# Kernel tuning notes

Measured on AMD Instinct MI355X. Metric: run time of the kernel, lower is better.

## Reference

```python
import jax, jax.numpy as jnp
import numpy as np

NUM_EMBEDDINGS = 8192
EMBEDDING_DIM = 256
COMMITMENT_COST = 0.25


def setup_inputs() -> dict:
    key = jax.random.key(0)
    k1, k2 = jax.random.split(key)
    z_e = jax.random.normal(k1, (16, 2048, EMBEDDING_DIM), dtype=jnp.float32)
    # nn.Embedding init: uniform(-1/K, 1/K)
    codebook = jax.random.uniform(
        k2, (NUM_EMBEDDINGS, EMBEDDING_DIM), dtype=jnp.float32,
        minval=-1.0 / NUM_EMBEDDINGS, maxval=1.0 / NUM_EMBEDDINGS)
    return {"z_e": z_e, "codebook": codebook}


def _nearest_indices(z_flat, codebook):
    # squared euclidean distances; argmin is identical to argmin of cdist
    # z_flat: [T, D], codebook: [K, D] -> dist2: [T, K]
    x2 = jnp.sum(z_flat * z_flat, axis=-1, keepdims=True)          # [T, 1]
    w2 = jnp.sum(codebook * codebook, axis=-1)                      # [K]
    xw = jnp.einsum('td,kd->tk', z_flat, codebook)                  # [T, K]
    dist2 = x2 - 2.0 * xw + w2
    return jnp.argmin(dist2, axis=1)                                # [T]


def reference(z_e, codebook):
    original_shape = z_e.shape
    z_e_flat = z_e.reshape(-1, EMBEDDING_DIM)
    indices = _nearest_indices(z_e_flat, codebook)
    z_q = codebook[indices].reshape(original_shape)
    # straight-through estimator
    z_q_ste = z_e + jax.lax.stop_gradient(z_q - z_e)
    commitment_loss = jnp.mean((z_e - jax.lax.stop_gradient(z_q_ste)) ** 2)
    codebook_loss = jnp.mean((z_q_ste - jax.lax.stop_gradient(z_e)) ** 2)
    loss = codebook_loss + COMMITMENT_COST * commitment_loss
    # codebook usage: fraction of unique indices (jit-friendly via scatter)
    used = jnp.zeros((NUM_EMBEDDINGS,), dtype=jnp.float32).at[indices].set(1.0)
    usage = jnp.sum(used) / NUM_EMBEDDINGS
    return (z_q_ste, loss, usage)
```

## Files before the change

### kernel.cpp

```cpp
#include <hip/hip_runtime.h>
#include <float.h>

#define T_TOTAL 32768
#define KC      8192
#define DIM     256

#define LOSS_IDX  ((size_t)T_TOTAL * DIM)
#define USAGE_IDX (LOSS_IDX + 1)

typedef short s16x8 __attribute__((ext_vector_type(8)));
typedef float f32x4 __attribute__((ext_vector_type(4)));

#define WS_W2    0
#define WS_FLAGS 32768
#define WS_CBF   65536

__device__ __forceinline__ unsigned short f2bf(float f) {
    unsigned int u = __float_as_uint(f);
    u += 0x7FFFu + ((u >> 16) & 1u);
    return (unsigned short)(u >> 16);
}

__global__ __launch_bounds__(256) void vq_prep(const float* __restrict__ cb,
                                               unsigned short* __restrict__ cbb,
                                               float* __restrict__ w2,
                                               int* __restrict__ flags,
                                               float* __restrict__ out) {
    const int blk = blockIdx.x, tid = threadIdx.x;
    size_t i = (size_t)blk * 2048 + (size_t)tid * 8;
    float4 a = *(const float4*)(cb + i);
    float4 b = *(const float4*)(cb + i + 4);
    uint4 o;
    o.x = (unsigned)f2bf(a.x) | ((unsigned)f2bf(a.y) << 16);
    o.y = (unsigned)f2bf(a.z) | ((unsigned)f2bf(a.w) << 16);
    o.z = (unsigned)f2bf(b.x) | ((unsigned)f2bf(b.y) << 16);
    o.w = (unsigned)f2bf(b.z) | ((unsigned)f2bf(b.w) << 16);
    *(uint4*)(cbb + i) = o;
    float s = a.x * a.x + a.y * a.y + a.z * a.z + a.w * a.w
            + b.x * b.x + b.y * b.y + b.z * b.z + b.w * b.w;
    #pragma unroll
    for (int m = 1; m <= 16; m <<= 1) s += __shfl_xor(s, m);
    if ((tid & 31) == 0) w2[blk * 8 + (tid >> 5)] = s;
    if (blk < 32) flags[blk * 256 + tid] = 0;
    if (blk == 0 && tid == 0) { out[LOSS_IDX] = 0.0f; out[USAGE_IDX] = 0.0f; }
}

__global__ __launch_bounds__(512, 2) void vq_main(const unsigned short* __restrict__ cbb,
                                                  const float* __restrict__ w2g,
                                                  const float* __restrict__ z_e,
                                                  const float* __restrict__ cb,
                                                  float* __restrict__ out,
                                                  int* __restrict__ flags) {
    __shared__ unsigned short ca[8][4][2048];
    __shared__ unsigned long long smin[128];
    __shared__ float wls[8];

    const int tid  = threadIdx.x;
    const int lane = tid & 63;
    const int w    = tid >> 6;
    const int wr   = w >> 2;
    const int wc   = w & 3;
    const int quad = lane >> 4;
    const int l15  = lane & 15;
    const int t0   = blockIdx.x * 128;

    if (tid < 128) smin[tid] = ~0ULL;
    __syncthreads();

    const int srow = lane >> 3;
    const int ssl  = lane & 7;
    const unsigned short* pstage = cbb + (wc * 32 + srow) * DIM + (ssl ^ srow) * 8;

    #define STAGE(PC, KW, BP)                                                           \
        {                                                                               \
            _Pragma("unroll")                                                           \
            for (int q = 0; q < 4; ++q) {                                               \
                __builtin_amdgcn_global_load_lds(                                       \
                    (const __attribute__((address_space(1))) void*)((PC) + (KW) * 64 + q * 2048), \
                    (__attribute__((address_space(3))) void*)(&ca[w][BP][q * 512]),     \
                    16, 0, 0);                                                          \
            }                                                                           \
        }

    const unsigned short* fragp[4];
    #pragma unroll
    for (int kk = 0; kk < 2; ++kk)
        #pragma unroll
        for (int j = 0; j < 2; ++j) {
            int row = j * 16 + l15;
            int sl = (kk * 4 + quad) ^ (l15 & 7);
            fragp[kk * 2 + j] = &ca[w][0][row * 64 + sl * 8];
        }

    #define READFRAGS(FB, BP)                                                           \
        {                                                                               \
            _Pragma("unroll")                                                           \
            for (int f = 0; f < 4; ++f)                                                 \
                (FB)[f] = *(const s16x8*)(fragp[f] + (BP) * 2048);                      \
        }

    STAGE(pstage, 0, 0); STAGE(pstage, 1, 1); STAGE(pstage, 2, 2); STAGE(pstage, 3, 3);
    s16x8 af[4][8];
    #pragma unroll
    for (int i = 0; i < 4; ++i) {
        #pragma unroll
        for (int ks = 0; ks < 8; ++ks) {
            const float* p = z_e + (size_t)(t0 + wr * 64 + i * 16 + l15) * DIM + ks * 32 + quad * 8;
            float4 a = *(const float4*)p;
            float4 b = *(const float4*)(p + 4);
            s16x8 v;
            v[0] = (short)f2bf(a.x); v[1] = (short)f2bf(a.y);
            v[2] = (short)f2bf(a.z); v[3] = (short)f2bf(a.w);
            v[4] = (short)f2bf(b.x); v[5] = (short)f2bf(b.y);
            v[6] = (short)f2bf(b.z); v[7] = (short)f2bf(b.w);
            af[i][ks] = v;
        }
    }

    float best[4][4];
    int   bidx[4][4];
    #pragma unroll
    for (int i = 0; i < 4; ++i)
        #pragma unroll
        for (int r = 0; r < 4; ++r) { best[i][r] = FLT_MAX; bidx[i][r] = 0x7FFFFFFF; }

    const float* pw2 = w2g + wc * 32 + l15;

    s16x8 regB[2][4];
    __builtin_amdgcn_s_waitcnt(0x0F7C);
    READFRAGS(regB[0], 0);

    for (int c = 0; c < 64; ++c) {
        f32x4 acc[4][2];
        #pragma unroll
        for (int i = 0; i < 4; ++i)
            #pragma unroll
            for (int j = 0; j < 2; ++j) acc[i][j] = (f32x4){0.f, 0.f, 0.f, 0.f};

        const unsigned short* pcn = pstage + ((size_t)((c + 1) & 63) << 15);

        #pragma unroll
        for (int kw = 0; kw < 4; ++kw) {
            __builtin_amdgcn_s_waitcnt(0xC07F);
            STAGE(pcn, kw, kw);
            __builtin_amdgcn_s_waitcnt(0x0F78);
            READFRAGS(regB[(kw + 1) & 1], (kw + 1) & 3);
            const s16x8* cur = regB[kw & 1];
            __builtin_amdgcn_s_setprio(1);
            #pragma unroll
            for (int kk = 0; kk < 2; ++kk)
                #pragma unroll
                for (int i = 0; i < 4; ++i)
                    #pragma unroll
                    for (int j = 0; j < 2; ++j)
                        acc[i][j] = __builtin_amdgcn_mfma_f32_16x16x32_bf16(af[i][kw * 2 + kk], cur[kk * 2 + j], acc[i][j], 0, 0, 0);
            __builtin_amdgcn_s_setprio(0);
        }

        #pragma unroll
        for (int j = 0; j < 2; ++j) {
            int col = c * 128 + wc * 32 + j * 16 + l15;
            float w2v = pw2[c * 128 + j * 16];
            #pragma unroll
            for (int i = 0; i < 4; ++i)
                #pragma unroll
                for (int r = 0; r < 4; ++r) {
                    float s = fmaf(-2.0f, acc[i][j][r], w2v);
                    if (s < best[i][r]) { best[i][r] = s; bidx[i][r] = col; }
                }
        }
    }

    #pragma unroll
    for (int i = 0; i < 4; ++i)
        #pragma unroll
        for (int r = 0; r < 4; ++r) {
            float b = best[i][r]; int ix = bidx[i][r];
            #pragma unroll
            for (int m = 1; m < 16; m <<= 1) {
                float ob = __shfl_xor(b, m);
                int   oi = __shfl_xor(ix, m);
                if (ob < b || (ob == b && oi < ix)) { b = ob; ix = oi; }
            }
            if (l15 == 0) {
                unsigned int fb = __float_as_uint(b);
                fb = (fb & 0x80000000u) ? ~fb : (fb | 0x80000000u);
                unsigned long long key = ((unsigned long long)fb << 32) | (unsigned int)ix;
                atomicMin(&smin[wr * 64 + i * 16 + quad * 4 + r], key);
            }
        }
    __syncthreads();

    float lsum = 0.0f;
    for (int t = w * 16; t < w * 16 + 16; ++t) {
        int tok = t0 + t;
        int k = (int)(unsigned int)(smin[t] & 0xFFFFFFFFull);
        if (lane == 0) flags[k] = 1;
        float4 cv = *(const float4*)(cb + (size_t)k * DIM + lane * 4);
        float4 zv = *(const float4*)(z_e + (size_t)tok * DIM + lane * 4);
        float dx = zv.x - cv.x, dy = zv.y - cv.y, dz = zv.z - cv.z, dw = zv.w - cv.w;
        lsum += dx * dx + dy * dy + dz * dz + dw * dw;
        *(float4*)(out + (size_t)tok * DIM + lane * 4) = cv;
    }
    #pragma unroll
    for (int m = 32; m >= 1; m >>= 1) lsum += __shfl_xor(lsum, m);
    if (lane == 0) wls[w] = lsum;
    __syncthreads();
    if (tid == 0) {
        float bsum = 0.0f;
        #pragma unroll
        for (int q = 0; q < 8; ++q) bsum += wls[q];
        atomicAdd(out + LOSS_IDX, bsum * (1.25f / (float)LOSS_IDX));
    }
}

__global__ __launch_bounds__(256) void vq_usage(const int* __restrict__ flags,
                                                float* __restrict__ out) {
    __shared__ int ws[4];
    int tid = threadIdx.x;
    int s = 0;
    for (int i = tid; i < KC; i += 256) s += flags[i];
    #pragma unroll
    for (int m = 32; m >= 1; m >>= 1) s += __shfl_xor(s, m);
    if ((tid & 63) == 0) ws[tid >> 6] = s;
    __syncthreads();
    if (tid == 0) out[USAGE_IDX] = (float)(ws[0] + ws[1] + ws[2] + ws[3]) / (float)KC;
}

extern "C" void kernel_launch(void* const* d_in, const int* in_sizes, int n_in,
                              void* d_out, int out_size, void* d_ws, size_t ws_size,
                              hipStream_t stream) {
    (void)in_sizes; (void)n_in; (void)out_size; (void)ws_size;
    const float* z_e = (const float*)d_in[0];
    const float* cb  = (const float*)d_in[1];
    float* out = (float*)d_out;

    char* ws = (char*)d_ws;
    float* w2    = (float*)(ws + WS_W2);
    int*   flags = (int*)(ws + WS_FLAGS);
    unsigned short* cbb = (unsigned short*)(ws + WS_CBF);

    vq_prep<<<KC / 8, 256, 0, stream>>>(cb, cbb, w2, flags, out);
    vq_main<<<T_TOTAL / 128, 512, 0, stream>>>(cbb, w2, z_e, cb, out, flags);
    vq_usage<<<1, 256, 0, stream>>>(flags, out);
}
```

Measured before the change: 243.1 us.

## Share codebook LDS tiles between wave pairs and cache w2 in shared memory

Waves with the same column group now load half of each codebook tile cooperatively into a shared LDS buffer, rather than every wave staging its own full copy. This halves global-to-LDS traffic and the LDS footprint. Block-wide barriers are added after every k-step so the shared buffers are not overwritten while still being read. The w2 norms for all codes are preloaded into LDS so per-chunk global loads disappear. The cost is a barrier per k-step, which can stall waves that would otherwise run independently.

```diff
diff --git a/kernel.cpp b/kernel.cpp
--- a/kernel.cpp
+++ b/kernel.cpp
@@ -51,7 +51,8 @@
                                                   const float* __restrict__ cb,
                                                   float* __restrict__ out,
                                                   int* __restrict__ flags) {
-    __shared__ unsigned short ca[8][4][2048];
+    __shared__ unsigned short ca[4][4][2048];
+    __shared__ float w2s[KC];
     __shared__ unsigned long long smin[128];
     __shared__ float wls[8];
 
@@ -65,21 +66,23 @@
     const int t0   = blockIdx.x * 128;
 
     if (tid < 128) smin[tid] = ~0ULL;
-    __syncthreads();
 
     const int srow = lane >> 3;
     const int ssl  = lane & 7;
-    const unsigned short* pstage = cbb + (wc * 32 + srow) * DIM + (ssl ^ srow) * 8;
+    const unsigned short* pstage =
+        cbb + (size_t)(wc * 32 + wr * 16 + srow) * DIM + (ssl ^ srow) * 8;
+    unsigned short* lb = &ca[wc][0][wr * 1024];
 
     #define STAGE(PC, KW, BP)                                                           \
         {                                                                               \
-            _Pragma("unroll")                                                           \
-            for (int q = 0; q < 4; ++q) {                                               \
-                __builtin_amdgcn_global_load_lds(                                       \
-                    (const __attribute__((address_space(1))) void*)((PC) + (KW) * 64 + q * 2048), \
-                    (__attribute__((address_space(3))) void*)(&ca[w][BP][q * 512]),     \
-                    16, 0, 0);                                                          \
-            }                                                                           \
+            __builtin_amdgcn_global_load_lds(                                           \
+                (const __attribute__((address_space(1))) void*)((PC) + (KW) * 64),      \
+                (__attribute__((address_space(3))) void*)(lb + (BP) * 2048),            \
+                16, 0, 0);                                                              \
+            __builtin_amdgcn_global_load_lds(                                           \
+                (const __attribute__((address_space(1))) void*)((PC) + (KW) * 64 + 2048), \
+                (__attribute__((address_space(3))) void*)(lb + (BP) * 2048 + 512),      \
+                16, 0, 0);                                                              \
         }
 
     const unsigned short* fragp[4];
@@ -89,7 +92,7 @@
         for (int j = 0; j < 2; ++j) {
             int row = j * 16 + l15;
             int sl = (kk * 4 + quad) ^ (l15 & 7);
-            fragp[kk * 2 + j] = &ca[w][0][row * 64 + sl * 8];
+            fragp[kk * 2 + j] = &ca[wc][0][row * 64 + sl * 8];
         }
 
     #define READFRAGS(FB, BP)                                                           \
@@ -100,6 +103,11 @@
         }
 
     STAGE(pstage, 0, 0); STAGE(pstage, 1, 1); STAGE(pstage, 2, 2); STAGE(pstage, 3, 3);
+    {
+        const float4* s = (const float4*)w2g + tid * 4;
+        float4* d = (float4*)w2s + tid * 4;
+        d[0] = s[0]; d[1] = s[1]; d[2] = s[2]; d[3] = s[3];
+    }
     s16x8 af[4][8];
     #pragma unroll
     for (int i = 0; i < 4; ++i) {
@@ -124,11 +132,14 @@
         #pragma unroll
         for (int r = 0; r < 4; ++r) { best[i][r] = FLT_MAX; bidx[i][r] = 0x7FFFFFFF; }
 
-    const float* pw2 = w2g + wc * 32 + l15;
+    const float* pw2s = &w2s[wc * 32 + l15];
 
     s16x8 regB[2][4];
-    __builtin_amdgcn_s_waitcnt(0x0F7C);
+    __builtin_amdgcn_s_waitcnt(0x0F70);
+    __syncthreads();
     READFRAGS(regB[0], 0);
+    __builtin_amdgcn_s_waitcnt(0xC07F);
+    __builtin_amdgcn_s_barrier();
 
     for (int c = 0; c < 64; ++c) {
         f32x4 acc[4][2];
@@ -141,9 +152,8 @@
 
         #pragma unroll
         for (int kw = 0; kw < 4; ++kw) {
-            __builtin_amdgcn_s_waitcnt(0xC07F);
             STAGE(pcn, kw, kw);
-            __builtin_amdgcn_s_waitcnt(0x0F78);
+            __builtin_amdgcn_s_waitcnt(0x0F74);
             READFRAGS(regB[(kw + 1) & 1], (kw + 1) & 3);
             const s16x8* cur = regB[kw & 1];
             __builtin_amdgcn_s_setprio(1);
@@ -155,12 +165,14 @@
                     for (int j = 0; j < 2; ++j)
                         acc[i][j] = __builtin_amdgcn_mfma_f32_16x16x32_bf16(af[i][kw * 2 + kk], cur[kk * 2 + j], acc[i][j], 0, 0, 0);
             __builtin_amdgcn_s_setprio(0);
+            __builtin_amdgcn_s_waitcnt(0xC07F);
+            __builtin_amdgcn_s_barrier();
         }
 
         #pragma unroll
         for (int j = 0; j < 2; ++j) {
             int col = c * 128 + wc * 32 + j * 16 + l15;
-            float w2v = pw2[c * 128 + j * 16];
+            float w2v = pw2s[c * 128 + j * 16];
             #pragma unroll
             for (int i = 0; i < 4; ++i)
                 #pragma unroll
```

New measurement: 253.5 us. 1.04x slower.

## Share staged codebook tiles across wave rows with block-level double buffering

Applied to the files above, without the earlier changes.

Previously each of the 8 waves staged its own private copy of the codebook tile, so the two waves sharing a column group loaded the same data twice. Now both wave rows cooperatively stage one shared tile per column group, which halves global-to-LDS traffic, and the buffer is double-buffered across chunks with a __syncthreads per chunk. The w2 loads are also hoisted to the start of each chunk. In exchange, the per-wave asynchronous pipeline is replaced by block-wide barriers, which can stall waves and reduce overlap between loads and MFMA work.

```diff
diff --git a/kernel.cpp b/kernel.cpp
--- a/kernel.cpp
+++ b/kernel.cpp
@@ -51,7 +51,7 @@
                                                   const float* __restrict__ cb,
                                                   float* __restrict__ out,
                                                   int* __restrict__ flags) {
-    __shared__ unsigned short ca[8][4][2048];
+    __shared__ unsigned short cs[4][2][8192];
     __shared__ unsigned long long smin[128];
     __shared__ float wls[8];
 
@@ -65,21 +65,25 @@
     const int t0   = blockIdx.x * 128;
 
     if (tid < 128) smin[tid] = ~0ULL;
-    __syncthreads();
 
     const int srow = lane >> 3;
     const int ssl  = lane & 7;
-    const unsigned short* pstage = cbb + (wc * 32 + srow) * DIM + (ssl ^ srow) * 8;
-
-    #define STAGE(PC, KW, BP)                                                           \
+    const unsigned short* pstage = cbb + (size_t)(wc * 32 + srow) * DIM + (ssl ^ srow) * 8;
+
+    #define STAGE(C, B)                                                                 \
         {                                                                               \
             _Pragma("unroll")                                                           \
-            for (int q = 0; q < 4; ++q) {                                               \
-                __builtin_amdgcn_global_load_lds(                                       \
-                    (const __attribute__((address_space(1))) void*)((PC) + (KW) * 64 + q * 2048), \
-                    (__attribute__((address_space(3))) void*)(&ca[w][BP][q * 512]),     \
-                    16, 0, 0);                                                          \
-            }                                                                           \
+            for (int kw = 0; kw < 4; ++kw)                                              \
+                _Pragma("unroll")                                                       \
+                for (int qq = 0; qq < 2; ++qq) {                                        \
+                    int q = wr * 2 + qq;                                                \
+                    __builtin_amdgcn_global_load_lds(                                   \
+                        (const __attribute__((address_space(1))) void*)                 \
+                            (pstage + (size_t)(C) * 32768 + q * 2048 + kw * 64),        \
+                        (__attribute__((address_space(3))) void*)                       \
+                            (&cs[wc][B][kw * 2048 + q * 512]),                          \
+                        16, 0, 0);                                                      \
+                }                                                                       \
         }
 
     const unsigned short* fragp[4];
@@ -89,17 +93,17 @@
         for (int j = 0; j < 2; ++j) {
             int row = j * 16 + l15;
             int sl = (kk * 4 + quad) ^ (l15 & 7);
-            fragp[kk * 2 + j] = &ca[w][0][row * 64 + sl * 8];
-        }
-
-    #define READFRAGS(FB, BP)                                                           \
+            fragp[kk * 2 + j] = &cs[wc][0][row * 64 + sl * 8];
+        }
+
+    #define READFRAGS(FB, B, KW)                                                        \
         {                                                                               \
             _Pragma("unroll")                                                           \
             for (int f = 0; f < 4; ++f)                                                 \
-                (FB)[f] = *(const s16x8*)(fragp[f] + (BP) * 2048);                      \
-        }
-
-    STAGE(pstage, 0, 0); STAGE(pstage, 1, 1); STAGE(pstage, 2, 2); STAGE(pstage, 3, 3);
+                (FB)[f] = *(const s16x8*)(fragp[f] + (B) * 8192 + (KW) * 2048);         \
+        }
+
+    STAGE(0, 0); STAGE(1, 1);
     s16x8 af[4][8];
     #pragma unroll
     for (int i = 0; i < 4; ++i) {
@@ -126,25 +130,24 @@
 
     const float* pw2 = w2g + wc * 32 + l15;
 
-    s16x8 regB[2][4];
-    __builtin_amdgcn_s_waitcnt(0x0F7C);
-    READFRAGS(regB[0], 0);
+    __builtin_amdgcn_s_waitcnt(0x0F70);
+    __syncthreads();
 
     for (int c = 0; c < 64; ++c) {
+        float w2a = pw2[c * 128];
+        float w2b = pw2[c * 128 + 16];
+
         f32x4 acc[4][2];
         #pragma unroll
         for (int i = 0; i < 4; ++i)
             #pragma unroll
             for (int j = 0; j < 2; ++j) acc[i][j] = (f32x4){0.f, 0.f, 0.f, 0.f};
 
-        const unsigned short* pcn = pstage + ((size_t)((c + 1) & 63) << 15);
-
+        s16x8 regB[2][4];
+        READFRAGS(regB[0], c & 1, 0);
         #pragma unroll
         for (int kw = 0; kw < 4; ++kw) {
-            __builtin_amdgcn_s_waitcnt(0xC07F);
-            STAGE(pcn, kw, kw);
-            __builtin_amdgcn_s_waitcnt(0x0F78);
-            READFRAGS(regB[(kw + 1) & 1], (kw + 1) & 3);
+            if (kw < 3) READFRAGS(regB[(kw + 1) & 1], c & 1, kw + 1);
             const s16x8* cur = regB[kw & 1];
             __builtin_amdgcn_s_setprio(1);
             #pragma unroll
@@ -160,7 +163,7 @@
         #pragma unroll
         for (int j = 0; j < 2; ++j) {
             int col = c * 128 + wc * 32 + j * 16 + l15;
-            float w2v = pw2[c * 128 + j * 16];
+            float w2v = j ? w2b : w2a;
             #pragma unroll
             for (int i = 0; i < 4; ++i)
                 #pragma unroll
@@ -169,6 +172,9 @@
                     if (s < best[i][r]) { best[i][r] = s; bidx[i][r] = col; }
                 }
         }
+
+        __syncthreads();
+        if (c < 62) STAGE(c + 2, c & 1);
     }
 
     #pragma unroll
```

Result: slower. 255.4 us (+5.0%).

## Stage codebook norms in LDS as bf16 and stagger chunk order per wave

Applied to the files above, without the earlier changes.

Codebook squared norms are now stored as bf16 and copied once per block into shared memory, so the inner loop reads them from LDS instead of global memory. Each wave also starts its sweep over codebook chunks at a different offset, which spreads global and L2 traffic across chunks. The argmin update gains a tie-break on lower index so results stay order-independent. Rounding norms to bf16 changes distance precision and may flip near-tie argmins; the extra LDS use may also affect occupancy.

```diff
diff --git a/kernel.cpp b/kernel.cpp
--- a/kernel.cpp
+++ b/kernel.cpp
@@ -23,7 +23,7 @@
 
 __global__ __launch_bounds__(256) void vq_prep(const float* __restrict__ cb,
                                                unsigned short* __restrict__ cbb,
-                                               float* __restrict__ w2,
+                                               unsigned short* __restrict__ w2,
                                                int* __restrict__ flags,
                                                float* __restrict__ out) {
     const int blk = blockIdx.x, tid = threadIdx.x;
@@ -40,18 +40,19 @@
             + b.x * b.x + b.y * b.y + b.z * b.z + b.w * b.w;
     #pragma unroll
     for (int m = 1; m <= 16; m <<= 1) s += __shfl_xor(s, m);
-    if ((tid & 31) == 0) w2[blk * 8 + (tid >> 5)] = s;
+    if ((tid & 31) == 0) w2[blk * 8 + (tid >> 5)] = f2bf(s);
     if (blk < 32) flags[blk * 256 + tid] = 0;
     if (blk == 0 && tid == 0) { out[LOSS_IDX] = 0.0f; out[USAGE_IDX] = 0.0f; }
 }
 
 __global__ __launch_bounds__(512, 2) void vq_main(const unsigned short* __restrict__ cbb,
-                                                  const float* __restrict__ w2g,
+                                                  const unsigned short* __restrict__ w2g,
                                                   const float* __restrict__ z_e,
                                                   const float* __restrict__ cb,
                                                   float* __restrict__ out,
                                                   int* __restrict__ flags) {
     __shared__ unsigned short ca[8][4][2048];
+    __shared__ unsigned short w2s[KC];
     __shared__ unsigned long long smin[128];
     __shared__ float wls[8];
 
@@ -63,13 +64,13 @@
     const int quad = lane >> 4;
     const int l15  = lane & 15;
     const int t0   = blockIdx.x * 128;
+    const int off  = (w * 8) & 63;
 
     if (tid < 128) smin[tid] = ~0ULL;
-    __syncthreads();
 
     const int srow = lane >> 3;
     const int ssl  = lane & 7;
-    const unsigned short* pstage = cbb + (wc * 32 + srow) * DIM + (ssl ^ srow) * 8;
+    const unsigned short* pstage = cbb + (size_t)(wc * 32 + srow) * DIM + (ssl ^ srow) * 8;
 
     #define STAGE(PC, KW, BP)                                                           \
         {                                                                               \
@@ -99,7 +100,15 @@
                 (FB)[f] = *(const s16x8*)(fragp[f] + (BP) * 2048);                      \
         }
 
-    STAGE(pstage, 0, 0); STAGE(pstage, 1, 1); STAGE(pstage, 2, 2); STAGE(pstage, 3, 3);
+    {
+        const uint4* s4 = (const uint4*)w2g;
+        uint4 v0 = s4[tid];
+        uint4 v1 = s4[tid + 512];
+        ((uint4*)w2s)[tid] = v0;
+        ((uint4*)w2s)[tid + 512] = v1;
+    }
+    const unsigned short* ps0 = pstage + ((size_t)off << 15);
+    STAGE(ps0, 0, 0); STAGE(ps0, 1, 1); STAGE(ps0, 2, 2); STAGE(ps0, 3, 3);
     s16x8 af[4][8];
     #pragma unroll
     for (int i = 0; i < 4; ++i) {
@@ -124,20 +133,20 @@
         #pragma unroll
         for (int r = 0; r < 4; ++r) { best[i][r] = FLT_MAX; bidx[i][r] = 0x7FFFFFFF; }
 
-    const float* pw2 = w2g + wc * 32 + l15;
-
     s16x8 regB[2][4];
-    __builtin_amdgcn_s_waitcnt(0x0F7C);
+    __builtin_amdgcn_s_waitcnt(0x0F70);
+    __syncthreads();
     READFRAGS(regB[0], 0);
 
     for (int c = 0; c < 64; ++c) {
+        const int gc = (c + off) & 63;
         f32x4 acc[4][2];
         #pragma unroll
         for (int i = 0; i < 4; ++i)
             #pragma unroll
             for (int j = 0; j < 2; ++j) acc[i][j] = (f32x4){0.f, 0.f, 0.f, 0.f};
 
-        const unsigned short* pcn = pstage + ((size_t)((c + 1) & 63) << 15);
+        const unsigned short* pcn = pstage + ((size_t)((c + 1 + off) & 63) << 15);
 
         #pragma unroll
         for (int kw = 0; kw < 4; ++kw) {
@@ -159,14 +168,16 @@
 
         #pragma unroll
         for (int j = 0; j < 2; ++j) {
-            int col = c * 128 + wc * 32 + j * 16 + l15;
-            float w2v = pw2[c * 128 + j * 16];
+            int col = gc * 128 + wc * 32 + j * 16 + l15;
+            float w2v = __uint_as_float((unsigned)w2s[col] << 16);
             #pragma unroll
             for (int i = 0; i < 4; ++i)
                 #pragma unroll
                 for (int r = 0; r < 4; ++r) {
                     float s = fmaf(-2.0f, acc[i][j][r], w2v);
-                    if (s < best[i][r]) { best[i][r] = s; bidx[i][r] = col; }
+                    if (s < best[i][r] || (s == best[i][r] && col < bidx[i][r])) {
+                        best[i][r] = s; bidx[i][r] = col;
+                    }
                 }
         }
     }
@@ -236,7 +247,7 @@
     float* out = (float*)d_out;
 
     char* ws = (char*)d_ws;
-    float* w2    = (float*)(ws + WS_W2);
+    unsigned short* w2  = (unsigned short*)(ws + WS_W2);
     int*   flags = (int*)(ws + WS_FLAGS);
     unsigned short* cbb = (unsigned short*)(ws + WS_CBF);
 
```

Measured after the change: 292.5 us. +20.3%, slower.
